# Kernel tuning notes

Measured on AMD Instinct MI355X. Metric: run time of the kernel, lower is better.

Reference implementation:

```python
import jax, jax.numpy as jnp
import numpy as np

B, N, CS, CZ, H, CH, G, P = 2, 384, 384, 128, 8, 16, 2, 8
CZ4 = CZ // 4
INF = 1e5
UMAX = 3.0     # self.u_max
LMAX = 2.0     # self.log_scale_max
SQRT_CH = CH ** 0.5


def quat_to_rot(q):
    q = q / jnp.linalg.norm(q, axis=-1, keepdims=True)
    w, x, y, z = q[..., 0], q[..., 1], q[..., 2], q[..., 3]
    R = jnp.stack([
        1 - 2 * (y * y + z * z), 2 * (x * y - w * z), 2 * (x * z + w * y),
        2 * (x * y + w * z), 1 - 2 * (x * x + z * z), 2 * (y * z - w * x),
        2 * (x * z - w * y), 2 * (y * z + w * x), 1 - 2 * (x * x + y * y)], axis=-1)
    return R.reshape(q.shape[:-1] + (3, 3))


def robust_nll(delta, sigma):
    # inline robust 3x3 Cholesky solve: dist_sq = d^T S^-1 d, log_det = ln|S|
    eps = 1e-8
    s00 = sigma[..., 0, 0]; s01 = sigma[..., 0, 1]; s02 = sigma[..., 0, 2]
    s11 = sigma[..., 1, 1]; s12 = sigma[..., 1, 2]; s22 = sigma[..., 2, 2]
    d0 = delta[..., 0]; d1 = delta[..., 1]; d2 = delta[..., 2]
    l00_sq = jnp.maximum(s00, eps); inv_l00 = jax.lax.rsqrt(l00_sq)
    l10 = s01 * inv_l00; l20 = s02 * inv_l00
    l11_sq = jnp.maximum(s11 - l10 * l10, eps); inv_l11 = jax.lax.rsqrt(l11_sq)
    l21 = (s12 - l20 * l10) * inv_l11
    l22_sq = jnp.maximum(s22 - l20 * l20 - l21 * l21, eps); inv_l22 = jax.lax.rsqrt(l22_sq)
    log_det = jnp.log(l00_sq) + jnp.log(l11_sq) + jnp.log(l22_sq)
    y0 = d0 * inv_l00
    y1 = (d1 - l10 * y0) * inv_l11
    y2 = (d2 - l20 * y0 - l21 * y1) * inv_l22
    return y0 * y0 + y1 * y1 + y2 * y2, log_det


def iga_forward(s, z, mask, rot, trans, local_mean, scaling_log,
                Wq, Wk, Wv, Wb, bb, Wdz, bdz, Wqg, bqg, Wkg, bkg,
                Wvp, bvp, geo_scale, geo_bias, Wout, bout):
    # scalar q/k/v: [B,H,N,CH]
    q = (s @ Wq).reshape(B, N, H, CH).transpose(0, 2, 1, 3)
    k = (s @ Wk).reshape(B, N, H, CH).transpose(0, 2, 1, 3)
    v = (s @ Wv).reshape(B, N, H, CH).transpose(0, 2, 1, 3)
    logits = jnp.einsum('bhid,bhjd->bhij', q, k) / SQRT_CH
    # pair bias: [B,H,N,N]
    logits = logits + (z @ Wb + bb).transpose(0, 3, 1, 2)

    def parse(feat):  # -> u [B,N,H,G,3], s_log_delta [B,N,H,G,3]
        raw = feat.reshape(B, N, H, G, 6)
        return jnp.tanh(raw[..., :3]) * UMAX, jnp.tanh(raw[..., 3:]) * LMAX

    def to_global(u, sld):
        anchor = local_mean[:, :, None, None, :]
        base = scaling_log[:, :, None, None, :]
        sig_loc = jnp.maximum(jnp.exp(base + sld), 1e-6)
        pos = anchor + u * sig_loc
        mu = jnp.einsum('bnij,bnhgj->bnhgi', rot, pos) + trans[:, :, None, None, :]
        var = jnp.exp(2.0 * (base + sld))
        Sig = jnp.einsum('bnij,bnhgj,bnkj->bnhgik', rot, var, rot)  # R diag(var) R^T
        return mu.transpose(0, 2, 1, 3, 4), Sig.transpose(0, 2, 1, 3, 4, 5)

    qu, qs = parse(s @ Wqg + bqg)
    ku, ks = parse(s @ Wkg + bkg)
    q_mu, q_sig = to_global(qu, qs)   # [B,H,N,G,3], [B,H,N,G,3,3]
    k_mu, k_sig = to_global(ku, ks)
    delta = q_mu[:, :, :, None] - k_mu[:, :, None, :]      # [B,H,N,N,G,3]
    ssum = q_sig[:, :, :, None] + k_sig[:, :, None, :]     # [B,H,N,N,G,3,3]
    dist_sq, log_det = robust_nll(delta, ssum)
    geo = (-0.5 * dist_sq - 0.5 * log_det).sum(-1)          # [B,H,N,N]

    mask2d = mask[:, None, :, None] * mask[:, None, None, :]  # [B,1,N,N]
    a = jax.nn.softplus(geo_scale)[None, :, None, None]
    G_geo = a * (geo * mask2d) + geo_bias[None, :, None, None]
    logits = logits + G_geo + (1.0 - mask2d) * (-INF)
    w = jax.nn.softmax(logits, axis=-1)                      # [B,H,N,N]

    # scalar output
    o = jnp.einsum('bhij,bhjd->bihd', w, v).reshape(B, N, H * CH)
    # point output (IPA-style): to global, attend, back to local frame
    vpts = (s @ Wvp + bvp).reshape(B, N, H, P, 3)
    vpg = jnp.einsum('bnij,bnhpj->bnhpi', rot, vpts) + trans[:, :, None, None, :]
    vpg = vpg.transpose(0, 2, 1, 3, 4)                       # [B,H,N,P,3]
    opt = jnp.einsum('bhij,bhjpc->bhipc', w, vpg)            # [B,H,N,P,3]
    opt_local = jnp.einsum('bnji,bhnpj->bnhpi', rot, opt - trans[:, None, :, None, :])
    onorm = jnp.sqrt((opt_local ** 2).sum(-1) + 1e-8)        # [B,N,H,P]
    # pair output
    pz = z @ Wdz + bdz                                       # [B,N,N,CZ4]
    opair = jnp.einsum('bhij,bijc->bihc', w, pz)             # [B,N,H,CZ4]

    cat = jnp.concatenate([o, opt_local.reshape(B, N, H * P * 3),
                           onorm.reshape(B, N, H * P),
                           opair.reshape(B, N, H * CZ4)], axis=-1)  # [B,N,640]
    return cat @ Wout + bout


def setup_inputs() -> dict:
    ks = jax.random.split(jax.random.key(0), 24)
    rnd = lambda i, shape, sc=1.0: jax.random.normal(ks[i], shape, dtype=jnp.float32) * sc
    w = 0.02
    return dict(
        s=rnd(0, (B, N, CS)), z=rnd(1, (B, N, N, CZ)),
        mask=jnp.ones((B, N), jnp.float32),
        rot=quat_to_rot(rnd(2, (B, N, 4))),
        trans=rnd(3, (B, N, 3), 1.0),
        local_mean=rnd(4, (B, N, 3), 0.5),
        scaling_log=rnd(5, (B, N, 3), 0.1),
        Wq=rnd(6, (CS, H * CH), w), Wk=rnd(7, (CS, H * CH), w), Wv=rnd(8, (CS, H * CH), w),
        Wb=rnd(9, (CZ, H), w), bb=rnd(10, (H,), w),
        Wdz=rnd(11, (CZ, CZ4), w), bdz=rnd(12, (CZ4,), w),
        Wqg=rnd(13, (CS, H * G * 6), w), bqg=rnd(14, (H * G * 6,), w),
        Wkg=rnd(15, (CS, H * G * 6), w), bkg=rnd(16, (H * G * 6,), w),
        Wvp=rnd(17, (CS, H * P * 3), w), bvp=rnd(18, (H * P * 3,), w),
        geo_scale=jnp.ones((H,), jnp.float32), geo_bias=jnp.zeros((H,), jnp.float32),
        Wout=rnd(19, (H * (CH + P * 4 + CZ4), CS), w), bout=jnp.zeros((CS,), jnp.float32))


def reference(s, z, mask, rot, trans, local_mean, scaling_log, Wq, Wk, Wv, Wb, bb,
              Wdz, bdz, Wqg, bqg, Wkg, bkg, Wvp, bvp, geo_scale, geo_bias, Wout, bout):
    return iga_forward(s, z, mask, rot, trans, local_mean, scaling_log, Wq, Wk, Wv,
                       Wb, bb, Wdz, bdz, Wqg, bqg, Wkg, bkg, Wvp, bvp,
                       geo_scale, geo_bias, Wout, bout)
```

## Files before the change

### kernel.cpp

```cpp
#include <hip/hip_runtime.h>
#include <hip/hip_fp16.h>

#define NB   2
#define NN   384
#define NCS  384
#define NCZ  128
#define NH   8
#define NCH  16
#define NG   2
#define NP   8
#define NCZ4 32
#define BN   (NB*NN)
#define LINW 768
#define PZROW ((size_t)BN*NN)
#define NZB  (BN*6)
#define NRB  288

typedef _Float16 f16x8 __attribute__((ext_vector_type(8)));
typedef float    f32x4 __attribute__((ext_vector_type(4)));

__global__ void k_wprep(const float* __restrict__ Wb, const float* __restrict__ Wdz,
                        _Float16* __restrict__ wf) {
    int t = threadIdx.x;
    for (int e = t; e < 12*64*8; e += 256) {
        int r = e & 7, lane = (e >> 3) & 63, nk = e >> 9;
        int n = nk >> 2, kk = nk & 3;
        int c = kk*32 + (lane >> 4)*8 + r;
        int col = n*16 + (lane & 15);
        float w;
        if      (col < 8)  w = Wb[c*NH + col];
        else if (col < 40) w = Wdz[c*NCZ4 + (col-8)];
        else               w = 0.f;
        wf[e] = (_Float16)w;
    }
}

__global__ void __launch_bounds__(256)
k_zrow(const float* __restrict__ z, const _Float16* __restrict__ wf,
       const float* __restrict__ bb, const float* __restrict__ bdz,
       const float* __restrict__ s,
       const float* __restrict__ Wq, const float* __restrict__ Wk,
       const float* __restrict__ Wv,
       const float* __restrict__ Wqg, const float* __restrict__ bqg,
       const float* __restrict__ Wkg, const float* __restrict__ bkg,
       const float* __restrict__ Wvp, const float* __restrict__ bvp,
       float* __restrict__ zbg, __half* __restrict__ pzg2,
       float* __restrict__ lin, float* __restrict__ kT, float* __restrict__ vT) {
    __shared__ __align__(16) char smem[12288];
    int t = threadIdx.x;

    if (blockIdx.x >= NRB) {
        float (*zbT)[64] = (float(*)[64])smem;
        __half (*pzt)[34] = (__half(*)[34])(smem + 2048);

        int lane = t & 63, w = t >> 6;
        int zb = blockIdx.x - NRB;
        int bi = zb / 6, ch = zb % 6;
        const float* zbase = z + ((size_t)bi*NN + ch*64)*NCZ;

        const float* ap = zbase + (size_t)(w*16 + (lane & 15))*NCZ + (lane >> 4)*8;
        float4 fa0a = *(const float4*)(ap +   0);
        float4 fa0b = *(const float4*)(ap +   4);
        float4 fa1a = *(const float4*)(ap +  32);
        float4 fa1b = *(const float4*)(ap +  36);
        float4 fa2a = *(const float4*)(ap +  64);
        float4 fa2b = *(const float4*)(ap +  68);
        float4 fa3a = *(const float4*)(ap +  96);
        float4 fa3b = *(const float4*)(ap + 100);

        f16x8 bfr[12];
        #pragma unroll
        for (int nk = 0; nk < 12; ++nk)
            bfr[nk] = ((const f16x8*)wf)[nk*64 + lane];

        int ccol = lane & 15;
        float b0 = (ccol < 8) ? bb[ccol] : bdz[ccol - 8];
        float b1 = bdz[ccol + 8];
        float b2 = (ccol < 8) ? bdz[ccol + 24] : 0.f;

        f16x8 af0, af1, af2, af3;
        af0[0]=(_Float16)fa0a.x; af0[1]=(_Float16)fa0a.y; af0[2]=(_Float16)fa0a.z; af0[3]=(_Float16)fa0a.w;
        af0[4]=(_Float16)fa0b.x; af0[5]=(_Float16)fa0b.y; af0[6]=(_Float16)fa0b.z; af0[7]=(_Float16)fa0b.w;
        af1[0]=(_Float16)fa1a.x; af1[1]=(_Float16)fa1a.y; af1[2]=(_Float16)fa1a.z; af1[3]=(_Float16)fa1a.w;
        af1[4]=(_Float16)fa1b.x; af1[5]=(_Float16)fa1b.y; af1[6]=(_Float16)fa1b.z; af1[7]=(_Float16)fa1b.w;
        af2[0]=(_Float16)fa2a.x; af2[1]=(_Float16)fa2a.y; af2[2]=(_Float16)fa2a.z; af2[3]=(_Float16)fa2a.w;
        af2[4]=(_Float16)fa2b.x; af2[5]=(_Float16)fa2b.y; af2[6]=(_Float16)fa2b.z; af2[7]=(_Float16)fa2b.w;
        af3[0]=(_Float16)fa3a.x; af3[1]=(_Float16)fa3a.y; af3[2]=(_Float16)fa3a.z; af3[3]=(_Float16)fa3a.w;
        af3[4]=(_Float16)fa3b.x; af3[5]=(_Float16)fa3b.y; af3[6]=(_Float16)fa3b.z; af3[7]=(_Float16)fa3b.w;

        int cjl = w*16 + (lane >> 4)*4;
        f32x4 ac0 = {0.f,0.f,0.f,0.f}, ac1 = ac0, ac2 = ac0;
        ac0 = __builtin_amdgcn_mfma_f32_16x16x32_f16(af0, bfr[0], ac0, 0,0,0);
        ac1 = __builtin_amdgcn_mfma_f32_16x16x32_f16(af0, bfr[4], ac1, 0,0,0);
        ac2 = __builtin_amdgcn_mfma_f32_16x16x32_f16(af0, bfr[8], ac2, 0,0,0);
        ac0 = __builtin_amdgcn_mfma_f32_16x16x32_f16(af1, bfr[1], ac0, 0,0,0);
        ac1 = __builtin_amdgcn_mfma_f32_16x16x32_f16(af1, bfr[5], ac1, 0,0,0);
        ac2 = __builtin_amdgcn_mfma_f32_16x16x32_f16(af1, bfr[9], ac2, 0,0,0);
        ac0 = __builtin_amdgcn_mfma_f32_16x16x32_f16(af2, bfr[2], ac0, 0,0,0);
        ac1 = __builtin_amdgcn_mfma_f32_16x16x32_f16(af2, bfr[6], ac1, 0,0,0);
        ac2 = __builtin_amdgcn_mfma_f32_16x16x32_f16(af2, bfr[10], ac2, 0,0,0);
        ac0 = __builtin_amdgcn_mfma_f32_16x16x32_f16(af3, bfr[3], ac0, 0,0,0);
        ac1 = __builtin_amdgcn_mfma_f32_16x16x32_f16(af3, bfr[7], ac1, 0,0,0);
        ac2 = __builtin_amdgcn_mfma_f32_16x16x32_f16(af3, bfr[11], ac2, 0,0,0);
        #pragma unroll
        for (int r = 0; r < 4; ++r) {
            int j = cjl + r;
            float v0 = ac0[r] + b0;
            if (ccol < 8) zbT[ccol][j] = v0;
            else          pzt[j][ccol-8] = __float2half(v0);
            pzt[j][ccol+8] = __float2half(ac1[r] + b1);
            if (ccol < 8)
                pzt[j][ccol+24] = __float2half(ac2[r] + b2);
        }
        __syncthreads();

        {
            int e = t*2, h = e >> 6, j = e & 63;
            float2 v; v.x = zbT[h][j]; v.y = zbT[h][j+1];
            *(float2*)(zbg + ((size_t)bi*NH + h)*NN + ch*64 + j) = v;
        }
        {
            int cp = t >> 4, l = t & 15, j0 = l*4;
            union { __half2 h2[4]; float4 f4; } u;
            #pragma unroll
            for (int r = 0; r < 4; ++r) {
                int j = j0 + r;
                u.h2[r] = __halves2half2(pzt[j][2*cp], pzt[j][2*cp+1]);
            }
            __half2* dst = (__half2*)pzg2 + (size_t)cp*PZROW + (size_t)bi*NN + ch*64 + j0;
            *(float4*)dst = u.f4;
        }
    } else {
        float (*sl)[NCS] = (float(*)[NCS])smem;
        int rb = blockIdx.x;
        int r0 = (rb / 3) * 8;
        int col = (rb % 3) * 256 + t;
        for (int idx = t; idx < 8*NCS; idx += 256)
            sl[idx / NCS][idx % NCS] = s[(size_t)(r0 + idx/NCS)*NCS + (idx % NCS)];
        __syncthreads();
        const float* W; int sw; float bias = 0.f;
        if      (col < 128) { W = Wq  + col;        sw = 128; }
        else if (col < 256) { W = Wk  + (col-128);  sw = 128; }
        else if (col < 384) { W = Wv  + (col-256);  sw = 128; }
        else if (col < 480) { W = Wqg + (col-384);  sw = 96;  bias = bqg[col-384]; }
        else if (col < 576) { W = Wkg + (col-480);  sw = 96;  bias = bkg[col-480]; }
        else                { W = Wvp + (col-576);  sw = 192; bias = bvp[col-576]; }
        float a[8];
        #pragma unroll
        for (int r = 0; r < 8; ++r) a[r] = 0.f;
        for (int c = 0; c < NCS; ++c) {
            float wv = W[(size_t)c*sw];
            #pragma unroll
            for (int r = 0; r < 8; ++r) a[r] = fmaf(sl[r][c], wv, a[r]);
        }
        #pragma unroll
        for (int r = 0; r < 8; ++r)
            lin[(size_t)(r0+r)*LINW + col] = a[r] + bias;
        if (col >= 128 && col < 384) {
            f32x4 v0, v1;
            #pragma unroll
            for (int r = 0; r < 4; ++r) { v0[r] = a[r]; v1[r] = a[4+r]; }
            float* dst = (col < 256) ? (kT + (size_t)(col-128)*BN + r0)
                                     : (vT + (size_t)(col-256)*BN + r0);
            *(f32x4*)dst = v0;
            *(f32x4*)(dst+4) = v1;
        }
    }
}

__global__ void k_geom(const float* __restrict__ lin, const float* __restrict__ rot,
                       const float* __restrict__ trans, const float* __restrict__ lm,
                       const float* __restrict__ sc,
                       float* __restrict__ qmu, float* __restrict__ qsig,
                       float* __restrict__ kmuT, float* __restrict__ ksigT,
                       float* __restrict__ vpgT) {
    int bn = blockIdx.x, t = threadIdx.x;
    __shared__ float R[9], T[3], A[3], Bs[3];
    if (t < 9) R[t] = rot[bn*9 + t];
    if (t < 3) { T[t] = trans[bn*3+t]; A[t] = lm[bn*3+t]; Bs[t] = sc[bn*3+t]; }
    __syncthreads();
    {
        int h = t >> 3, p = t & 7;
        const float* vr = lin + (size_t)bn*LINW + 576 + h*24 + p*3;
        float x = vr[0], y = vr[1], z = vr[2];
        int e = h*24 + p*3;
        vpgT[(size_t)(e+0)*BN + bn] = R[0]*x + R[1]*y + R[2]*z + T[0];
        vpgT[(size_t)(e+1)*BN + bn] = R[3]*x + R[4]*y + R[5]*z + T[1];
        vpgT[(size_t)(e+2)*BN + bn] = R[6]*x + R[7]*y + R[8]*z + T[2];
    }
    if (t < 32) {
        int side = t >> 4, item = t & 15;
        const float* raw = lin + (size_t)bn*LINW + (side ? 480 : 384) + item*6;
        float u0 = tanhf(raw[0])*3.f, u1 = tanhf(raw[1])*3.f, u2 = tanhf(raw[2])*3.f;
        float e0 = Bs[0] + tanhf(raw[3])*2.f;
        float e1 = Bs[1] + tanhf(raw[4])*2.f;
        float e2 = Bs[2] + tanhf(raw[5])*2.f;
        float sl0 = fmaxf(expf(e0), 1e-6f);
        float sl1 = fmaxf(expf(e1), 1e-6f);
        float sl2 = fmaxf(expf(e2), 1e-6f);
        float p0 = A[0] + u0*sl0, p1 = A[1] + u1*sl1, p2 = A[2] + u2*sl2;
        float mu0 = R[0]*p0 + R[1]*p1 + R[2]*p2 + T[0];
        float mu1 = R[3]*p0 + R[4]*p1 + R[5]*p2 + T[1];
        float mu2 = R[6]*p0 + R[7]*p1 + R[8]*p2 + T[2];
        float v0 = expf(2.f*e0), v1 = expf(2.f*e1), v2 = expf(2.f*e2);
        float s00 = R[0]*R[0]*v0 + R[1]*R[1]*v1 + R[2]*R[2]*v2;
        float s01 = R[0]*R[3]*v0 + R[1]*R[4]*v1 + R[2]*R[5]*v2;
        float s02 = R[0]*R[6]*v0 + R[1]*R[7]*v1 + R[2]*R[8]*v2;
        float s11 = R[3]*R[3]*v0 + R[4]*R[4]*v1 + R[5]*R[5]*v2;
        float s12 = R[3]*R[6]*v0 + R[4]*R[7]*v1 + R[5]*R[8]*v2;
        float s22 = R[6]*R[6]*v0 + R[7]*R[7]*v1 + R[8]*R[8]*v2;
        if (side) {
            kmuT[(size_t)(item*3+0)*BN + bn] = mu0;
            kmuT[(size_t)(item*3+1)*BN + bn] = mu1;
            kmuT[(size_t)(item*3+2)*BN + bn] = mu2;
            ksigT[(size_t)(item*6+0)*BN + bn] = s00;
            ksigT[(size_t)(item*6+1)*BN + bn] = s01;
            ksigT[(size_t)(item*6+2)*BN + bn] = s02;
            ksigT[(size_t)(item*6+3)*BN + bn] = s11;
            ksigT[(size_t)(item*6+4)*BN + bn] = s12;
            ksigT[(size_t)(item*6+5)*BN + bn] = s22;
        } else {
            float* mud = qmu + (size_t)bn*48 + item*3;
            mud[0]=mu0; mud[1]=mu1; mud[2]=mu2;
            float* sgd = qsig + (size_t)bn*96 + item*6;
            sgd[0]=s00; sgd[1]=s01; sgd[2]=s02; sgd[3]=s11; sgd[4]=s12; sgd[5]=s22;
        }
    }
}

__global__ void __launch_bounds__(256, 2)
k_attn2(const float* __restrict__ mask,
        const float* __restrict__ rot, const float* __restrict__ trans,
        const float* __restrict__ lin,
        const float* __restrict__ qmu, const float* __restrict__ qsig,
        const float* __restrict__ kmuT, const float* __restrict__ ksigT,
        const float* __restrict__ kT, const float* __restrict__ vT,
        const float* __restrict__ vpgT,
        const float* __restrict__ zbg, const __half* __restrict__ pzg2,
        const float* __restrict__ gsc, const float* __restrict__ gbi,
        float* __restrict__ cat) {
    __shared__ float  logits[NH][NN];
    __shared__ float  qrow[128];
    __shared__ float  qmu_s[48], qsig_s[96];
    __shared__ float  Rm[9], Tv[3];
    __shared__ float  aH[NH], bH[NH];
    __shared__ float  maskI;

    int t  = threadIdx.x;
    int b  = blockIdx.x / NN, i = blockIdx.x % NN;
    int bi = b*NN + i;
    const size_t boff = (size_t)b*NN;

    if (t < 128) qrow[t] = lin[(size_t)bi*LINW + t];
    if (t < 48)  qmu_s[t] = qmu[(size_t)bi*48 + t];
    if (t >= 64 && t < 160) qsig_s[t-64] = qsig[(size_t)bi*96 + (t-64)];
    if (t >= 160 && t < 169) Rm[t-160] = rot[bi*9 + (t-160)];
    if (t >= 169 && t < 172) Tv[t-169] = trans[bi*3 + (t-169)];
    if (t >= 176 && t < 184) {
        int h = t-176;
        float x = gsc[h];
        aH[h] = (x > 20.f) ? x : log1pf(expf(x));
        bH[h] = gbi[h];
    }
    if (t == 255) maskI = mask[bi];
    __syncthreads();

    int h = t >> 5, lnn = t & 31;
    {
        float qv[16];
        #pragma unroll
        for (int d = 0; d < 16; ++d) qv[d] = qrow[h*16 + d];
        float qm[6], qs[12];
        #pragma unroll
        for (int e = 0; e < 6; ++e)  qm[e] = qmu_s[h*6 + e];
        #pragma unroll
        for (int e = 0; e < 12; ++e) qs[e] = qsig_s[h*12 + e];
        float ascale = aH[h], hbias = bH[h], mI = maskI;
        #pragma unroll 1
        for (int jj = 0; jj < 3; ++jj) {
            int j4 = jj*128 + lnn*4;
            const float* kp = kT + (size_t)(h*16)*BN + boff + j4;
            f32x4 qk = {0.f,0.f,0.f,0.f};
            #pragma unroll
            for (int d = 0; d < 16; ++d) {
                f32x4 kv = *(const f32x4*)(kp + (size_t)d*BN);
                #pragma unroll
                for (int r = 0; r < 4; ++r) qk[r] = fmaf(qv[d], kv[r], qk[r]);
            }
            f32x4 geo = {0.f,0.f,0.f,0.f};
            #pragma unroll
            for (int g = 0; g < NG; ++g) {
                const float* kmb = kmuT + (size_t)((h*2+g)*3)*BN + boff + j4;
                f32x4 km0 = *(const f32x4*)(kmb);
                f32x4 km1 = *(const f32x4*)(kmb + BN);
                f32x4 km2 = *(const f32x4*)(kmb + 2*BN);
                const float* ksb = ksigT + (size_t)((h*2+g)*6)*BN + boff + j4;
                f32x4 ks0 = *(const f32x4*)(ksb);
                f32x4 ks1 = *(const f32x4*)(ksb + BN);
                f32x4 ks2 = *(const f32x4*)(ksb + 2*BN);
                f32x4 ks3 = *(const f32x4*)(ksb + 3*BN);
                f32x4 ks4 = *(const f32x4*)(ksb + 4*BN);
                f32x4 ks5 = *(const f32x4*)(ksb + 5*BN);
                #pragma unroll
                for (int r = 0; r < 4; ++r) {
                    float d0 = qm[g*3+0] - km0[r];
                    float d1 = qm[g*3+1] - km1[r];
                    float d2 = qm[g*3+2] - km2[r];
                    float s00 = qs[g*6+0] + ks0[r];
                    float s01 = qs[g*6+1] + ks1[r];
                    float s02 = qs[g*6+2] + ks2[r];
                    float s11 = qs[g*6+3] + ks3[r];
                    float s12 = qs[g*6+4] + ks4[r];
                    float s22 = qs[g*6+5] + ks5[r];
                    float l00 = fmaxf(s00, 1e-8f);
                    float i00 = rsqrtf(l00);
                    float l10 = s01*i00, l20 = s02*i00;
                    float l11 = fmaxf(s11 - l10*l10, 1e-8f);
                    float i11 = rsqrtf(l11);
                    float l21 = (s12 - l20*l10)*i11;
                    float l22 = fmaxf(s22 - l20*l20 - l21*l21, 1e-8f);
                    float i22 = rsqrtf(l22);
                    float ld = __logf(l00) + __logf(l11) + __logf(l22);
                    float y0 = d0*i00;
                    float y1 = (d1 - l10*y0)*i11;
                    float y2 = (d2 - l20*y0 - l21*y1)*i22;
                    geo[r] += -0.5f*(y0*y0 + y1*y1 + y2*y2 + ld);
                }
            }
            f32x4 zb4 = *(const f32x4*)(zbg + ((size_t)bi*NH + h)*NN + j4);
            f32x4 mv  = *(const f32x4*)(mask + boff + j4);
            f32x4 lg;
            #pragma unroll
            for (int r = 0; r < 4; ++r) {
                float m2 = mI * mv[r];
                lg[r] = qk[r]*0.25f + zb4[r] + ascale*(geo[r]*m2) + hbias
                        + (1.f - m2)*(-100000.f);
            }
            *(f32x4*)&logits[h][j4] = lg;
        }
    }
    __syncthreads();

    float mx = -3.4e38f;
    #pragma unroll
    for (int jj = 0; jj < 12; ++jj) mx = fmaxf(mx, logits[h][lnn + jj*32]);
    #pragma unroll
    for (int m = 16; m >= 1; m >>= 1) mx = fmaxf(mx, __shfl_xor(mx, m, 64));
    float se = 0.f;
    #pragma unroll
    for (int jj = 0; jj < 12; ++jj) {
        int j = lnn + jj*32;
        float e = __expf(logits[h][j] - mx);
        logits[h][j] = e;
        se += e;
    }
    #pragma unroll
    for (int m = 16; m >= 1; m >>= 1) se += __shfl_xor(se, m, 64);
    float inv = 1.f / se;
    float* cp = cat + (size_t)bi*640;

    {
        float o[16];
        #pragma unroll
        for (int d = 0; d < 16; ++d) o[d] = 0.f;
        const float* vbase = vT + (size_t)(h*16)*BN + boff;
        #pragma unroll 1
        for (int jj = 0; jj < 3; ++jj) {
            int j4 = jj*128 + lnn*4;
            f32x4 lg4 = *(const f32x4*)&logits[h][j4];
            f32x4 w4;
            #pragma unroll
            for (int r = 0; r < 4; ++r) w4[r] = lg4[r] * inv;
            const float* vb = vbase + j4;
            #pragma unroll
            for (int d = 0; d < 16; ++d) {
                f32x4 kv = *(const f32x4*)(vb + (size_t)d*BN);
                #pragma unroll
                for (int r = 0; r < 4; ++r) o[d] = fmaf(w4[r], kv[r], o[d]);
            }
        }
        #pragma unroll
        for (int m = 16; m >= 1; m >>= 1) {
            #pragma unroll
            for (int d = 0; d < 16; ++d) o[d] += __shfl_xor(o[d], m, 64);
        }
        if (lnn == 0) {
            #pragma unroll
            for (int d = 0; d < 16; ++d) cp[h*16 + d] = o[d];
        }
    }

    {
        float op[24];
        #pragma unroll
        for (int e = 0; e < 24; ++e) op[e] = 0.f;
        const float* gbase = vpgT + (size_t)(h*24)*BN + boff;
        #pragma unroll 1
        for (int jj = 0; jj < 3; ++jj) {
            int j4 = jj*128 + lnn*4;
            f32x4 lg4 = *(const f32x4*)&logits[h][j4];
            f32x4 w4;
            #pragma unroll
            for (int r = 0; r < 4; ++r) w4[r] = lg4[r] * inv;
            const float* gb = gbase + j4;
            #pragma unroll
            for (int e = 0; e < 24; ++e) {
                f32x4 gv = *(const f32x4*)(gb + (size_t)e*BN);
                #pragma unroll
                for (int r = 0; r < 4; ++r) op[e] = fmaf(w4[r], gv[r], op[e]);
            }
        }
        #pragma unroll
        for (int m = 16; m >= 1; m >>= 1) {
            #pragma unroll
            for (int e = 0; e < 24; ++e) op[e] += __shfl_xor(op[e], m, 64);
        }
        if (lnn == 0) {
            #pragma unroll
            for (int p = 0; p < 8; ++p) {
                float x  = op[p*3+0] - Tv[0];
                float y  = op[p*3+1] - Tv[1];
                float zz = op[p*3+2] - Tv[2];
                float l0 = Rm[0]*x + Rm[3]*y + Rm[6]*zz;
                float l1 = Rm[1]*x + Rm[4]*y + Rm[7]*zz;
                float l2 = Rm[2]*x + Rm[5]*y + Rm[8]*zz;
                cp[128 + h*24 + p*3 + 0] = l0;
                cp[128 + h*24 + p*3 + 1] = l1;
                cp[128 + h*24 + p*3 + 2] = l2;
                cp[320 + h*8 + p] = sqrtf(l0*l0 + l1*l1 + l2*l2 + 1e-8f);
            }
        }
    }

    {
        float opa[32];
        #pragma unroll
        for (int c = 0; c < 32; ++c) opa[c] = 0.f;
        const __half2* pzb = (const __half2*)pzg2 + (size_t)bi*NN;
        #pragma unroll 1
        for (int jj = 0; jj < 3; ++jj) {
            int j4 = jj*128 + lnn*4;
            f32x4 lg4 = *(const f32x4*)&logits[h][j4];
            f32x4 w4;
            #pragma unroll
            for (int r = 0; r < 4; ++r) w4[r] = lg4[r] * inv;
            #pragma unroll
            for (int c2 = 0; c2 < 16; ++c2) {
                union { float4 f4; __half2 h2[4]; } u;
                u.f4 = *(const float4*)(pzb + (size_t)c2*PZROW + j4);
                #pragma unroll
                for (int r = 0; r < 4; ++r) {
                    float2 pf = __half22float2(u.h2[r]);
                    opa[2*c2]   = fmaf(w4[r], pf.x, opa[2*c2]);
                    opa[2*c2+1] = fmaf(w4[r], pf.y, opa[2*c2+1]);
                }
            }
        }
        #pragma unroll
        for (int m = 16; m >= 1; m >>= 1) {
            #pragma unroll
            for (int c = 0; c < 32; ++c) opa[c] += __shfl_xor(opa[c], m, 64);
        }
        if (lnn == 0) {
            #pragma unroll
            for (int c = 0; c < 32; ++c) cp[384 + h*32 + c] = opa[c];
        }
    }
}

__global__ void k_out(const float* __restrict__ cat, const float* __restrict__ Wout,
                      const float* __restrict__ bout, float* __restrict__ out) {
    __shared__ float cl[4][640];
    int t  = threadIdx.x;
    int r0 = blockIdx.x * 4;
    for (int idx = t; idx < 4*640; idx += 384)
        cl[idx/640][idx%640] = cat[(size_t)(r0 + idx/640)*640 + (idx%640)];
    __syncthreads();
    int col = t;
    float a0=0.f, a1=0.f, a2=0.f, a3=0.f;
    for (int c = 0; c < 640; ++c) {
        float w = Wout[(size_t)c*NCS + col];
        a0 = fmaf(cl[0][c], w, a0);
        a1 = fmaf(cl[1][c], w, a1);
        a2 = fmaf(cl[2][c], w, a2);
        a3 = fmaf(cl[3][c], w, a3);
    }
    float bv = bout[col];
    out[(size_t)(r0+0)*NCS + col] = a0 + bv;
    out[(size_t)(r0+1)*NCS + col] = a1 + bv;
    out[(size_t)(r0+2)*NCS + col] = a2 + bv;
    out[(size_t)(r0+3)*NCS + col] = a3 + bv;
}

extern "C" void kernel_launch(void* const* d_in, const int* in_sizes, int n_in,
                              void* d_out, int out_size, void* d_ws, size_t ws_size,
                              hipStream_t stream) {
    const float* s    = (const float*)d_in[0];
    const float* z    = (const float*)d_in[1];
    const float* mask = (const float*)d_in[2];
    const float* rot  = (const float*)d_in[3];
    const float* trans= (const float*)d_in[4];
    const float* lm   = (const float*)d_in[5];
    const float* sc   = (const float*)d_in[6];
    const float* Wq   = (const float*)d_in[7];
    const float* Wk   = (const float*)d_in[8];
    const float* Wv   = (const float*)d_in[9];
    const float* Wb   = (const float*)d_in[10];
    const float* bb   = (const float*)d_in[11];
    const float* Wdz  = (const float*)d_in[12];
    const float* bdz  = (const float*)d_in[13];
    const float* Wqg  = (const float*)d_in[14];
    const float* bqg  = (const float*)d_in[15];
    const float* Wkg  = (const float*)d_in[16];
    const float* bkg  = (const float*)d_in[17];
    const float* Wvp  = (const float*)d_in[18];
    const float* bvp  = (const float*)d_in[19];
    const float* gsc  = (const float*)d_in[20];
    const float* gbi  = (const float*)d_in[21];
    const float* Wout = (const float*)d_in[22];
    const float* bout = (const float*)d_in[23];
    float* out = (float*)d_out;

    float* ws    = (float*)d_ws;
    float* lin   = ws;
    float* qmu   = lin   + 589824;
    float* qsig  = qmu   + 36864;
    float* kmuT  = qsig  + 73728;
    float* ksigT = kmuT  + 36864;
    float* vpgT  = ksigT + 73728;
    float* kT    = vpgT  + 147456;
    float* vT    = kT    + 98304;
    float* cat   = vT    + 98304;
    float* zbg   = cat   + 491520;
    __half* pzg2 = (__half*)(zbg + 2359296);
    _Float16* wf = (_Float16*)((float*)pzg2 + 4718592);

    k_wprep<<<1, 256, 0, stream>>>(Wb, Wdz, wf);
    k_zrow<<<NZB + NRB, 256, 0, stream>>>(z, wf, bb, bdz, s,
                                          Wq, Wk, Wv, Wqg, bqg, Wkg, bkg, Wvp, bvp,
                                          zbg, pzg2, lin, kT, vT);
    k_geom<<<BN, 64, 0, stream>>>(lin, rot, trans, lm, sc, qmu, qsig, kmuT, ksigT, vpgT);
    k_attn2<<<BN, 256, 0, stream>>>(mask, rot, trans, lin, qmu, qsig, kmuT, ksigT,
                                    kT, vT, vpgT, zbg, pzg2, gsc, gbi, cat);
    k_out<<<192, 384, 0, stream>>>(cat, Wout, bout, out);
}
```

Before: 150.1 us.

## Make z-projection blocks loop over chunks with register prefetch and double-buffered LDS

The z pair-projection part of k_zrow now launches 1152 blocks instead of 4608. Each block processes four 64-row chunks in a loop. While the MFMA work and stores for the current chunk run, the next chunk's z values are prefetched into registers, and the LDS staging alternates between two buffers so each iteration needs only one barrier. The aim is to hide global-load latency on this bandwidth-heavy stream and to amortise the per-block weight-fragment and bias loads across chunks. The explicit 256-thread launch bound was dropped, which may change how the compiler allocates registers, and the larger register footprint from prefetching can lower occupancy.

```diff
diff --git a/kernel.cpp b/kernel.cpp
--- a/kernel.cpp
+++ b/kernel.cpp
@@ -13,7 +13,8 @@
 #define BN   (NB*NN)
 #define LINW 768
 #define PZROW ((size_t)BN*NN)
-#define NZB  (BN*6)
+#define NCHUNK (BN*6)
+#define NZP  1152
 #define NRB  288
 
 typedef _Float16 f16x8 __attribute__((ext_vector_type(8)));
@@ -35,8 +36,7 @@
     }
 }
 
-__global__ void __launch_bounds__(256)
-k_zrow(const float* __restrict__ z, const _Float16* __restrict__ wf,
+__global__ void k_zrow(const float* __restrict__ z, const _Float16* __restrict__ wf,
        const float* __restrict__ bb, const float* __restrict__ bdz,
        const float* __restrict__ s,
        const float* __restrict__ Wq, const float* __restrict__ Wk,
@@ -46,89 +46,107 @@
        const float* __restrict__ Wvp, const float* __restrict__ bvp,
        float* __restrict__ zbg, __half* __restrict__ pzg2,
        float* __restrict__ lin, float* __restrict__ kT, float* __restrict__ vT) {
-    __shared__ __align__(16) char smem[12288];
+    __shared__ __align__(16) char smem[12800];
     int t = threadIdx.x;
 
     if (blockIdx.x >= NRB) {
-        float (*zbT)[64] = (float(*)[64])smem;
-        __half (*pzt)[34] = (__half(*)[34])(smem + 2048);
-
         int lane = t & 63, w = t >> 6;
-        int zb = blockIdx.x - NRB;
-        int bi = zb / 6, ch = zb % 6;
-        const float* zbase = z + ((size_t)bi*NN + ch*64)*NCZ;
-
-        const float* ap = zbase + (size_t)(w*16 + (lane & 15))*NCZ + (lane >> 4)*8;
-        float4 fa0a = *(const float4*)(ap +   0);
-        float4 fa0b = *(const float4*)(ap +   4);
-        float4 fa1a = *(const float4*)(ap +  32);
-        float4 fa1b = *(const float4*)(ap +  36);
-        float4 fa2a = *(const float4*)(ap +  64);
-        float4 fa2b = *(const float4*)(ap +  68);
-        float4 fa3a = *(const float4*)(ap +  96);
-        float4 fa3b = *(const float4*)(ap + 100);
+        int ccol = lane & 15;
+        int cjl  = w*16 + (lane >> 4)*4;
+        int zbid = blockIdx.x - NRB;
 
         f16x8 bfr[12];
         #pragma unroll
         for (int nk = 0; nk < 12; ++nk)
             bfr[nk] = ((const f16x8*)wf)[nk*64 + lane];
 
-        int ccol = lane & 15;
         float b0 = (ccol < 8) ? bb[ccol] : bdz[ccol - 8];
         float b1 = bdz[ccol + 8];
         float b2 = (ccol < 8) ? bdz[ccol + 24] : 0.f;
 
-        f16x8 af0, af1, af2, af3;
-        af0[0]=(_Float16)fa0a.x; af0[1]=(_Float16)fa0a.y; af0[2]=(_Float16)fa0a.z; af0[3]=(_Float16)fa0a.w;
-        af0[4]=(_Float16)fa0b.x; af0[5]=(_Float16)fa0b.y; af0[6]=(_Float16)fa0b.z; af0[7]=(_Float16)fa0b.w;
-        af1[0]=(_Float16)fa1a.x; af1[1]=(_Float16)fa1a.y; af1[2]=(_Float16)fa1a.z; af1[3]=(_Float16)fa1a.w;
-        af1[4]=(_Float16)fa1b.x; af1[5]=(_Float16)fa1b.y; af1[6]=(_Float16)fa1b.z; af1[7]=(_Float16)fa1b.w;
-        af2[0]=(_Float16)fa2a.x; af2[1]=(_Float16)fa2a.y; af2[2]=(_Float16)fa2a.z; af2[3]=(_Float16)fa2a.w;
-        af2[4]=(_Float16)fa2b.x; af2[5]=(_Float16)fa2b.y; af2[6]=(_Float16)fa2b.z; af2[7]=(_Float16)fa2b.w;
-        af3[0]=(_Float16)fa3a.x; af3[1]=(_Float16)fa3a.y; af3[2]=(_Float16)fa3a.z; af3[3]=(_Float16)fa3a.w;
-        af3[4]=(_Float16)fa3b.x; af3[5]=(_Float16)fa3b.y; af3[6]=(_Float16)fa3b.z; af3[7]=(_Float16)fa3b.w;
-
-        int cjl = w*16 + (lane >> 4)*4;
-        f32x4 ac0 = {0.f,0.f,0.f,0.f}, ac1 = ac0, ac2 = ac0;
-        ac0 = __builtin_amdgcn_mfma_f32_16x16x32_f16(af0, bfr[0], ac0, 0,0,0);
-        ac1 = __builtin_amdgcn_mfma_f32_16x16x32_f16(af0, bfr[4], ac1, 0,0,0);
-        ac2 = __builtin_amdgcn_mfma_f32_16x16x32_f16(af0, bfr[8], ac2, 0,0,0);
-        ac0 = __builtin_amdgcn_mfma_f32_16x16x32_f16(af1, bfr[1], ac0, 0,0,0);
-        ac1 = __builtin_amdgcn_mfma_f32_16x16x32_f16(af1, bfr[5], ac1, 0,0,0);
-        ac2 = __builtin_amdgcn_mfma_f32_16x16x32_f16(af1, bfr[9], ac2, 0,0,0);
-        ac0 = __builtin_amdgcn_mfma_f32_16x16x32_f16(af2, bfr[2], ac0, 0,0,0);
-        ac1 = __builtin_amdgcn_mfma_f32_16x16x32_f16(af2, bfr[6], ac1, 0,0,0);
-        ac2 = __builtin_amdgcn_mfma_f32_16x16x32_f16(af2, bfr[10], ac2, 0,0,0);
-        ac0 = __builtin_amdgcn_mfma_f32_16x16x32_f16(af3, bfr[3], ac0, 0,0,0);
-        ac1 = __builtin_amdgcn_mfma_f32_16x16x32_f16(af3, bfr[7], ac1, 0,0,0);
-        ac2 = __builtin_amdgcn_mfma_f32_16x16x32_f16(af3, bfr[11], ac2, 0,0,0);
-        #pragma unroll
-        for (int r = 0; r < 4; ++r) {
-            int j = cjl + r;
-            float v0 = ac0[r] + b0;
-            if (ccol < 8) zbT[ccol][j] = v0;
-            else          pzt[j][ccol-8] = __float2half(v0);
-            pzt[j][ccol+8] = __float2half(ac1[r] + b1);
-            if (ccol < 8)
-                pzt[j][ccol+24] = __float2half(ac2[r] + b2);
-        }
-        __syncthreads();
-
+        int c = zbid;
+        float4 pre[8];
         {
-            int e = t*2, h = e >> 6, j = e & 63;
-            float2 v; v.x = zbT[h][j]; v.y = zbT[h][j+1];
-            *(float2*)(zbg + ((size_t)bi*NH + h)*NN + ch*64 + j) = v;
-        }
-        {
-            int cp = t >> 4, l = t & 15, j0 = l*4;
-            union { __half2 h2[4]; float4 f4; } u;
+            const float* ap = z + ((size_t)(c/6)*NN + (c%6)*64)*NCZ
+                            + (size_t)(w*16 + (lane & 15))*NCZ + (lane >> 4)*8;
+            #pragma unroll
+            for (int kk = 0; kk < 4; ++kk) {
+                pre[2*kk+0] = *(const float4*)(ap + kk*32);
+                pre[2*kk+1] = *(const float4*)(ap + kk*32 + 4);
+            }
+        }
+
+        #pragma unroll 1
+        for (int it = 0; it < 4; ++it) {
+            int bi = c / 6, ch = c % 6;
+            char* buf = smem + (it & 1) * 6400;
+            float (*zbT)[64] = (float(*)[64])buf;
+            __half (*pzt)[34] = (__half(*)[34])(buf + 2048);
+
+            f16x8 af0, af1, af2, af3;
+            af0[0]=(_Float16)pre[0].x; af0[1]=(_Float16)pre[0].y; af0[2]=(_Float16)pre[0].z; af0[3]=(_Float16)pre[0].w;
+            af0[4]=(_Float16)pre[1].x; af0[5]=(_Float16)pre[1].y; af0[6]=(_Float16)pre[1].z; af0[7]=(_Float16)pre[1].w;
+            af1[0]=(_Float16)pre[2].x; af1[1]=(_Float16)pre[2].y; af1[2]=(_Float16)pre[2].z; af1[3]=(_Float16)pre[2].w;
+            af1[4]=(_Float16)pre[3].x; af1[5]=(_Float16)pre[3].y; af1[6]=(_Float16)pre[3].z; af1[7]=(_Float16)pre[3].w;
+            af2[0]=(_Float16)pre[4].x; af2[1]=(_Float16)pre[4].y; af2[2]=(_Float16)pre[4].z; af2[3]=(_Float16)pre[4].w;
+            af2[4]=(_Float16)pre[5].x; af2[5]=(_Float16)pre[5].y; af2[6]=(_Float16)pre[5].z; af2[7]=(_Float16)pre[5].w;
+            af3[0]=(_Float16)pre[6].x; af3[1]=(_Float16)pre[6].y; af3[2]=(_Float16)pre[6].z; af3[3]=(_Float16)pre[6].w;
+            af3[4]=(_Float16)pre[7].x; af3[5]=(_Float16)pre[7].y; af3[6]=(_Float16)pre[7].z; af3[7]=(_Float16)pre[7].w;
+
+            if (it < 3) {
+                int cn = c + NZP;
+                const float* ap = z + ((size_t)(cn/6)*NN + (cn%6)*64)*NCZ
+                                + (size_t)(w*16 + (lane & 15))*NCZ + (lane >> 4)*8;
+                #pragma unroll
+                for (int kk = 0; kk < 4; ++kk) {
+                    pre[2*kk+0] = *(const float4*)(ap + kk*32);
+                    pre[2*kk+1] = *(const float4*)(ap + kk*32 + 4);
+                }
+            }
+
+            f32x4 ac0 = {0.f,0.f,0.f,0.f}, ac1 = ac0, ac2 = ac0;
+            ac0 = __builtin_amdgcn_mfma_f32_16x16x32_f16(af0, bfr[0], ac0, 0,0,0);
+            ac1 = __builtin_amdgcn_mfma_f32_16x16x32_f16(af0, bfr[4], ac1, 0,0,0);
+            ac2 = __builtin_amdgcn_mfma_f32_16x16x32_f16(af0, bfr[8], ac2, 0,0,0);
+            ac0 = __builtin_amdgcn_mfma_f32_16x16x32_f16(af1, bfr[1], ac0, 0,0,0);
+            ac1 = __builtin_amdgcn_mfma_f32_16x16x32_f16(af1, bfr[5], ac1, 0,0,0);
+            ac2 = __builtin_amdgcn_mfma_f32_16x16x32_f16(af1, bfr[9], ac2, 0,0,0);
+            ac0 = __builtin_amdgcn_mfma_f32_16x16x32_f16(af2, bfr[2], ac0, 0,0,0);
+            ac1 = __builtin_amdgcn_mfma_f32_16x16x32_f16(af2, bfr[6], ac1, 0,0,0);
+            ac2 = __builtin_amdgcn_mfma_f32_16x16x32_f16(af2, bfr[10], ac2, 0,0,0);
+            ac0 = __builtin_amdgcn_mfma_f32_16x16x32_f16(af3, bfr[3], ac0, 0,0,0);
+            ac1 = __builtin_amdgcn_mfma_f32_16x16x32_f16(af3, bfr[7], ac1, 0,0,0);
+            ac2 = __builtin_amdgcn_mfma_f32_16x16x32_f16(af3, bfr[11], ac2, 0,0,0);
+
             #pragma unroll
             for (int r = 0; r < 4; ++r) {
-                int j = j0 + r;
-                u.h2[r] = __halves2half2(pzt[j][2*cp], pzt[j][2*cp+1]);
-            }
-            __half2* dst = (__half2*)pzg2 + (size_t)cp*PZROW + (size_t)bi*NN + ch*64 + j0;
-            *(float4*)dst = u.f4;
+                int j = cjl + r;
+                float v0 = ac0[r] + b0;
+                if (ccol < 8) zbT[ccol][j] = v0;
+                else          pzt[j][ccol-8] = __float2half(v0);
+                pzt[j][ccol+8] = __float2half(ac1[r] + b1);
+                if (ccol < 8)
+                    pzt[j][ccol+24] = __float2half(ac2[r] + b2);
+            }
+            __syncthreads();
+
+            {
+                int e = t*2, h = e >> 6, j = e & 63;
+                float2 v; v.x = zbT[h][j]; v.y = zbT[h][j+1];
+                *(float2*)(zbg + ((size_t)bi*NH + h)*NN + ch*64 + j) = v;
+            }
+            {
+                int cp = t >> 4, l = t & 15, j0 = l*4;
+                union { __half2 h2[4]; float4 f4; } u;
+                #pragma unroll
+                for (int r = 0; r < 4; ++r) {
+                    int j = j0 + r;
+                    u.h2[r] = __halves2half2(pzt[j][2*cp], pzt[j][2*cp+1]);
+                }
+                __half2* dst = (__half2*)pzg2 + (size_t)cp*PZROW + (size_t)bi*NN + ch*64 + j0;
+                *(float4*)dst = u.f4;
+            }
+            c += NZP;
         }
     } else {
         float (*sl)[NCS] = (float(*)[NCS])smem;
@@ -536,7 +554,7 @@
     _Float16* wf = (_Float16*)((float*)pzg2 + 4718592);
 
     k_wprep<<<1, 256, 0, stream>>>(Wb, Wdz, wf);
-    k_zrow<<<NZB + NRB, 256, 0, stream>>>(z, wf, bb, bdz, s,
+    k_zrow<<<NRB + NZP, 256, 0, stream>>>(z, wf, bb, bdz, s,
                                           Wq, Wk, Wv, Wqg, bqg, Wkg, bkg, Wvp, bvp,
                                           zbg, pzg2, lin, kT, vT);
     k_geom<<<BN, 64, 0, stream>>>(lin, rot, trans, lm, sc, qmu, qsig, kmuT, ksigT, vpgT);
```

New measurement: 151.5 us. About the same (+0.9%).
